# Kernel tuning notes

Measured on AMD Instinct MI355X. Metric: run time of the kernel, lower is better.

## Reference

```python
import jax, jax.numpy as jnp
import numpy as np

TAU = 0.2
ALPHA = 0.8
EPS = 1e-8  # torch cosine_similarity eps
LAM_POS = 1.5  # generate_lambda()=0.5, +1 for extrapolation
LAM_NEG = 0.5  # interpolation lambda


def _cos_sim_matrix(x):
    # row-normalize with clamped norm (matches F.cosine_similarity eps), then gram matrix
    n = x / jnp.maximum(jnp.linalg.norm(x, axis=1, keepdims=True), EPS)
    return n @ n.T


def setup_inputs() -> dict:
    key = jax.random.key(0)
    N, D = 4096, 512
    emb = jax.random.normal(key, (N, D), dtype=jnp.float32)
    # SimCLR-style symmetric positive pairs: (2k,2k+1) and (2k+1,2k)
    base = np.arange(0, N, 2)
    fwd_pairs = np.stack([base, base + 1], axis=1)
    pairs = np.concatenate([fwd_pairs, fwd_pairs[:, ::-1]], axis=0)  # [N, 2]
    return {"embeddings": emb, "positive_pairs": jnp.asarray(pairs, dtype=jnp.int32)}


def reference(embeddings, positive_pairs):
    # stage == 'train' (quantile-thresholded hard-negative branch)
    N = embeddings.shape[0]
    ar = jnp.arange(N)
    pi, pj = positive_pairs[:, 0], positive_pairs[:, 1]
    # ordered positive mask (symmetric because pairs include both orientations)
    pos_mask = jnp.zeros((N, N), dtype=bool).at[pi, pj].set(True)

    # --- extrapolate positive pairs: row i -> 1.5*e_i - 0.5*e_j ---
    partner_pos = jnp.full((N,), -1, dtype=jnp.int32).at[pi].set(pj.astype(jnp.int32))
    in_pair = partner_pos >= 0
    pp = jnp.where(in_pair, partner_pos, 0)
    hard_pos_emb = jnp.where(
        in_pair[:, None],
        LAM_POS * embeddings - (LAM_POS - 1.0) * embeddings[pp],
        embeddings,
    )

    # --- interpolate negative pairs: row k -> 0.5*(e_k + e_partner) ---
    # Negative pairs are all ordered (i,j), i!=j, not positive, scattered in
    # row k is the largest i with (i,k) negative.
    valid = (~pos_mask.T) & (ar[None, :] != ar[:, None])  # valid[k, i] = (i,k) is negative
    partner_neg = jnp.max(jnp.where(valid, ar[None, :], -1), axis=1)
    hard_neg_emb = LAM_NEG * embeddings + (1.0 - LAM_NEG) * embeddings[partner_neg]

    # --- three NxN cosine-sim matrices, composed by the scatter pattern ---
    orig_sim = _cos_sim_matrix(embeddings)
    hard_pos_sim = _cos_sim_matrix(hard_pos_emb)
    hard_neg_sim = _cos_sim_matrix(hard_neg_emb)
    diag = jnp.eye(N, dtype=bool)
    sim = jnp.where(diag, orig_sim, jnp.where(pos_mask, hard_pos_sim, hard_neg_sim))

    # --- contrastive loss with per-row quantile hard-negative threshold ---
    mask = diag | pos_mask
    exp_sim = jnp.exp(sim / TAU)
    exp_masked = jnp.where(mask, 0.0, exp_sim)
    pos_sim = exp_sim[pi, pj]              # [P]
    exp_rows = exp_masked[pi]              # [P, N]
    thr = jnp.quantile(exp_rows, ALPHA, axis=1, keepdims=True)
    hard_neg_sum = jnp.sum(jnp.where(exp_rows >= thr, exp_rows, 0.0), axis=1)
    loss = -jnp.log(pos_sim / (pos_sim + hard_neg_sum))
    # torch sums loss_ij + loss_ji over all rows / (2*P); with symmetric pair
    # list this equals sum(loss_ij)/P
    return jnp.sum(loss) / positive_pairs.shape[0]
```

## Files before the change

### kernel.cpp

```cpp
#include <hip/hip_runtime.h>
#include <cmath>

#define DIM 512
#define TAU_INV 5.0f
#define EPSN 1e-8f
#define ALPHA_Q 0.8f

typedef __attribute__((ext_vector_type(8))) unsigned short us8;
typedef __attribute__((ext_vector_type(4))) unsigned short us4;
typedef __attribute__((ext_vector_type(8))) short s8v;
typedef __attribute__((ext_vector_type(4))) float f4;

__device__ __forceinline__ unsigned short f2h(float f) {
    _Float16 h = (_Float16)f;
    return *(const unsigned short*)&h;
}
__device__ __forceinline__ float h2f(unsigned u) {
    unsigned short us = (unsigned short)u;
    _Float16 h = *(const _Float16*)&us;
    return (float)h;
}
__device__ __forceinline__ unsigned key16(unsigned u) {
    return u ^ (0x8000u | (0x7FFFu & (0u - (u >> 15))));
}
__device__ __forceinline__ float keyval(unsigned k) {
    unsigned u = (k & 0x8000u) ? (k & 0x7FFFu) : ((~k) & 0xFFFFu);
    return h2f(u);
}

__global__ void k_scatter(const int* __restrict__ pairs, int* partner, int P) {
    int k = blockIdx.x * 256 + threadIdx.x;
    if (k < P) partner[pairs[2 * k]] = pairs[2 * k + 1];
}
__global__ void k_pneg(const int* __restrict__ partner, int* pneg, int N) {
    int i = blockIdx.x * 256 + threadIdx.x;
    if (i >= N) return;
    int q = -1;
    for (int j = N - 1; j >= 0; --j) {
        if (j != i && partner[j] != i) { q = j; break; }
    }
    pneg[i] = q;
}

__global__ __launch_bounds__(128) void k_prep(const float* __restrict__ emb,
                                              const int* __restrict__ pneg,
                                              const int* __restrict__ pairs,
                                              unsigned short* __restrict__ mb,
                                              float* __restrict__ pos_term,
                                              int N, int P) {
    int bid = blockIdx.x, t = threadIdx.x;
    if (bid < N) {
        int i = bid;
        int q = pneg[i];
        float4 a = ((const float4*)(emb + (size_t)i * DIM))[t];
        float4 b = ((const float4*)(emb + (size_t)q * DIM))[t];
        float hx = 0.5f * (a.x + b.x), hy = 0.5f * (a.y + b.y);
        float hz = 0.5f * (a.z + b.z), hw = 0.5f * (a.w + b.w);
        float ss = hx * hx + hy * hy + hz * hz + hw * hw;
        for (int o = 32; o > 0; o >>= 1) ss += __shfl_down(ss, o);
        __shared__ float red[2];
        __shared__ float s_inv;
        if ((t & 63) == 0) red[t >> 6] = ss;
        __syncthreads();
        if (t == 0) s_inv = 1.0f / fmaxf(sqrtf(red[0] + red[1]), EPSN);
        __syncthreads();
        float inv = s_inv;
        us4 o4;
        o4[0] = f2h(hx * inv); o4[1] = f2h(hy * inv);
        o4[2] = f2h(hz * inv); o4[3] = f2h(hw * inv);
        *(us4*)(mb + (size_t)i * DIM + t * 4) = o4;
    } else {
        int k = bid - N;
        int i = pairs[2 * k], j = pairs[2 * k + 1];
        float4 a = ((const float4*)(emb + (size_t)i * DIM))[t];
        float4 b = ((const float4*)(emb + (size_t)j * DIM))[t];
        float dab = 0.f, naa = 0.f, nbb = 0.f;
        {
            float fa, fb;
            fa = 1.5f * a.x - 0.5f * b.x; fb = 1.5f * b.x - 0.5f * a.x; dab += fa * fb; naa += fa * fa; nbb += fb * fb;
            fa = 1.5f * a.y - 0.5f * b.y; fb = 1.5f * b.y - 0.5f * a.y; dab += fa * fb; naa += fa * fa; nbb += fb * fb;
            fa = 1.5f * a.z - 0.5f * b.z; fb = 1.5f * b.z - 0.5f * a.z; dab += fa * fb; naa += fa * fa; nbb += fb * fb;
            fa = 1.5f * a.w - 0.5f * b.w; fb = 1.5f * b.w - 0.5f * a.w; dab += fa * fb; naa += fa * fa; nbb += fb * fb;
        }
        for (int o = 32; o > 0; o >>= 1) {
            dab += __shfl_down(dab, o);
            naa += __shfl_down(naa, o);
            nbb += __shfl_down(nbb, o);
        }
        __shared__ float rd[2], ra[2], rb[2];
        if ((t & 63) == 0) { rd[t >> 6] = dab; ra[t >> 6] = naa; rb[t >> 6] = nbb; }
        __syncthreads();
        if (t == 0) {
            float d = rd[0] + rd[1], na = ra[0] + ra[1], nb = rb[0] + rb[1];
            float sim = d / (fmaxf(sqrtf(na), EPSN) * fmaxf(sqrtf(nb), EPSN));
            pos_term[k] = expf(sim * TAU_INV);
        }
    }
}

__global__ __launch_bounds__(256) void k_gemm(const unsigned short* __restrict__ mb,
                                              unsigned short* __restrict__ S, int N, int rowBase) {
    __shared__ __align__(16) unsigned short As[128][32];
    __shared__ __align__(16) unsigned short Bs[128][32];
    int tid = threadIdx.x;
    int wave = tid >> 6, lane = tid & 63, quad = lane >> 4, l16 = lane & 15;
    int wr = (wave >> 1) * 64, wc = (wave & 1) * 64;
    int iBase = rowBase + blockIdx.y * 128;
    int jBase = blockIdx.x * 128;
    int lrow = lane >> 2, lseg = lane & 3;

    const unsigned short* gA0 = mb + (size_t)(iBase + wave * 32 + lrow) * DIM + lseg * 8;
    const unsigned short* gA1 = gA0 + 16 * DIM;
    const unsigned short* gB0 = mb + (size_t)(jBase + wave * 32 + lrow) * DIM + lseg * 8;
    const unsigned short* gB1 = gB0 + 16 * DIM;
    __attribute__((address_space(3))) char* ldsA =
        (__attribute__((address_space(3))) char*)As + wave * 2048;
    __attribute__((address_space(3))) char* ldsB =
        (__attribute__((address_space(3))) char*)Bs + wave * 2048;

    f4 acc[4][4];
    for (int i = 0; i < 4; ++i)
        for (int j = 0; j < 4; ++j) acc[i][j] = (f4){0.f, 0.f, 0.f, 0.f};

    for (int k0 = 0; k0 < DIM; k0 += 32) {
        __syncthreads();
        __builtin_amdgcn_global_load_lds(
            (const __attribute__((address_space(1))) void*)(gA0 + k0),
            (__attribute__((address_space(3))) void*)(ldsA), 16, 0, 0);
        __builtin_amdgcn_global_load_lds(
            (const __attribute__((address_space(1))) void*)(gA1 + k0),
            (__attribute__((address_space(3))) void*)(ldsA + 1024), 16, 0, 0);
        __builtin_amdgcn_global_load_lds(
            (const __attribute__((address_space(1))) void*)(gB0 + k0),
            (__attribute__((address_space(3))) void*)(ldsB), 16, 0, 0);
        __builtin_amdgcn_global_load_lds(
            (const __attribute__((address_space(1))) void*)(gB1 + k0),
            (__attribute__((address_space(3))) void*)(ldsB + 1024), 16, 0, 0);
        __syncthreads();

        s8v a[4], b[4];
        for (int i = 0; i < 4; ++i) a[i] = *(const s8v*)&As[wr + i * 16 + l16][quad * 8];
        for (int j = 0; j < 4; ++j) b[j] = *(const s8v*)&Bs[wc + j * 16 + l16][quad * 8];
        for (int i = 0; i < 4; ++i)
            for (int j = 0; j < 4; ++j)
                acc[i][j] = __builtin_amdgcn_mfma_f32_16x16x32_f16(a[i], b[j], acc[i][j], 0, 0, 0);
    }
    int rQ = blockIdx.y * 128 + wr + quad * 4;
    int cQ = jBase + wc + l16;
    for (int i = 0; i < 4; ++i)
        for (int j = 0; j < 4; ++j)
            for (int rr = 0; rr < 4; ++rr)
                S[(size_t)(rQ + i * 16 + rr) * N + cQ + j * 16] = f2h(acc[i][j][rr]);
}

__global__ __launch_bounds__(256, 4) void k_select(const unsigned short* __restrict__ Sb,
                                                   const int* __restrict__ pairs,
                                                   const float* __restrict__ pos_term,
                                                   float* __restrict__ losses,
                                                   int N, int r0, int r1,
                                                   int klo, float frac) {
    __shared__ unsigned shcnt[2];
    __shared__ unsigned shmin;
    __shared__ float s_red[4];
    int tid = threadIdx.x, wid = tid >> 6, lane = tid & 63;
    int k = blockIdx.x;
    int row = pairs[2 * k];
    if (row < r0 || row >= r1) return;
    int pj = pairs[2 * k + 1];
    const us8* src8 = (const us8*)(Sb + (size_t)(row - r0) * N);

    us8 g0 = src8[tid];
    us8 g1 = src8[256 + tid];
    unsigned kr[16];
    {
        int m0 = row - tid * 8, p0 = pj - tid * 8;
        int m1 = row - 2048 - tid * 8, p1 = pj - 2048 - tid * 8;
        #pragma unroll
        for (int e = 0; e < 8; ++e) {
            unsigned u = (unsigned short)g0[e];
            kr[e] = ((e == m0) | (e == p0)) ? 0u : key16(u);
        }
        #pragma unroll
        for (int e = 0; e < 8; ++e) {
            unsigned u = (unsigned short)g1[e];
            kr[8 + e] = ((e == m1) | (e == p1)) ? 0u : key16(u);
        }
    }

    int nmask = (pj == row) ? 1 : 2;
    int Nreal = N - nmask;
    int Rreal = klo - nmask;
    float pos = pos_term[k];
    float s = 0.f;

    if (Rreal < 0) {
        #pragma unroll
        for (int e = 0; e < 16; ++e)
            if (kr[e] > 0u) s += __expf(keyval(kr[e]) * TAU_INV);
    } else {
        if (tid < 2) shcnt[tid] = 0u;
        if (tid == 0) shmin = 0xFFFFFFFFu;
        __syncthreads();
        int lim = Nreal - Rreal - 1;
        unsigned lo = 1, hi = 65535;
        int parity = 0;
        while (lo < hi) {
            unsigned mid = (lo + hi) >> 1;
            unsigned wcnt = 0;
            #pragma unroll
            for (int e = 0; e < 16; ++e)
                wcnt += (unsigned)__popcll(__ballot(kr[e] > mid));
            if (lane == 0) atomicAdd(&shcnt[parity], wcnt);
            __syncthreads();
            unsigned cnt = shcnt[parity];
            if (tid == 0) shcnt[parity ^ 1] = 0u;
            __syncthreads();
            if (cnt <= (unsigned)lim) hi = mid; else lo = mid + 1;
            parity ^= 1;
        }
        unsigned K1 = lo;

        if (frac > 1e-9f) {
            unsigned wcnt = 0, mymin = 0xFFFFFFFFu;
            #pragma unroll
            for (int e = 0; e < 16; ++e) {
                bool gt = kr[e] > K1;
                wcnt += (unsigned)__popcll(__ballot(gt));
                if (gt && kr[e] < mymin) mymin = kr[e];
            }
            for (int o = 1; o < 64; o <<= 1) {
                unsigned y = (unsigned)__shfl_xor((int)mymin, o);
                if (y < mymin) mymin = y;
            }
            if (lane == 0) {
                atomicAdd(&shcnt[parity], wcnt);
                atomicMin(&shmin, mymin);
            }
            __syncthreads();
            unsigned cntAbove = shcnt[parity];
            unsigned minAbove = shmin;
            unsigned K2;
            if (Rreal + 1 > Nreal - 1)                K2 = K1;
            else if (Nreal - (int)cntAbove >= Rreal + 2) K2 = K1;
            else                                      K2 = minAbove;
            float elo = __expf(keyval(K1) * TAU_INV);
            float ehi = __expf(keyval(K2) * TAU_INV);
            float thr = elo + frac * (ehi - elo);
            #pragma unroll
            for (int e = 0; e < 16; ++e) {
                if (kr[e] > 0u) {
                    float ev = __expf(keyval(kr[e]) * TAU_INV);
                    if (ev >= thr) s += ev;
                }
            }
        } else {
            #pragma unroll
            for (int e = 0; e < 16; ++e)
                if (kr[e] >= K1) s += __expf(keyval(kr[e]) * TAU_INV);
        }
    }

    for (int o = 1; o < 64; o <<= 1) s += __shfl_xor(s, o);
    if (lane == 0) s_red[wid] = s;
    __syncthreads();
    if (tid == 0) {
        float st = s_red[0] + s_red[1] + s_red[2] + s_red[3];
        losses[k] = logf((pos + st) / pos);
    }
}

__global__ __launch_bounds__(256) void k_reduce(const float* __restrict__ losses,
                                                float* __restrict__ out, int P, float invP) {
    __shared__ float s_red[4];
    int tid = threadIdx.x, wid = tid >> 6, lane = tid & 63;
    float s = 0.f;
    for (int i = tid; i < P; i += 256) s += losses[i];
    for (int o = 1; o < 64; o <<= 1) s += __shfl_xor(s, o);
    if (lane == 0) s_red[wid] = s;
    __syncthreads();
    if (tid == 0) out[0] = (s_red[0] + s_red[1] + s_red[2] + s_red[3]) * invP;
}

extern "C" void kernel_launch(void* const* d_in, const int* in_sizes, int n_in,
                              void* d_out, int out_size, void* d_ws, size_t ws_size,
                              hipStream_t stream) {
    const float* emb = (const float*)d_in[0];
    const int* pairs = (const int*)d_in[1];
    float* out = (float*)d_out;
    int N = in_sizes[0] / DIM;
    int P = in_sizes[1] / 2;

    char* ws = (char*)d_ws;
    size_t off = 0;
    unsigned short* mb = (unsigned short*)(ws + off); off += (size_t)N * DIM * 2;
    int* partner = (int*)(ws + off);                  off += (size_t)N * 4;
    int* pneg = (int*)(ws + off);                     off += (size_t)N * 4;
    float* pos_term = (float*)(ws + off);             off += (size_t)P * 4;
    float* losses = (float*)(ws + off);               off += (size_t)P * 4;
    off = (off + 255) & ~(size_t)255;
    unsigned short* Sbuf = (unsigned short*)(ws + off);
    size_t avail = (ws_size > off) ? ws_size - off : 0;
    long maxRows = (long)(avail / ((size_t)N * 2));
    int chunk = (int)(maxRows - (maxRows % 128));
    if (chunk > N) chunk = N;
    if (chunk < 128) chunk = 128;

    hipMemsetAsync(partner, 0xFF, (size_t)N * 4, stream);
    k_scatter<<<dim3((P + 255) / 256), dim3(256), 0, stream>>>(pairs, partner, P);
    k_pneg<<<dim3((N + 255) / 256), dim3(256), 0, stream>>>(partner, pneg, N);
    k_prep<<<dim3(N + P), dim3(128), 0, stream>>>(emb, pneg, pairs, mb, pos_term, N, P);

    float qpos = ALPHA_Q * (float)(N - 1);
    int klo = (int)floorf(qpos);
    float frac = qpos - (float)klo;
    float invP = 1.0f / (float)P;

    for (int r0 = 0; r0 < N; r0 += chunk) {
        int rows = (N - r0 < chunk) ? (N - r0) : chunk;
        dim3 g(N / 128, rows / 128);
        k_gemm<<<g, dim3(256), 0, stream>>>(mb, Sbuf, N, r0);
        k_select<<<dim3(P), dim3(256), 0, stream>>>(Sbuf, pairs, pos_term, losses,
                                                    N, r0, r0 + rows, klo, frac);
    }
    k_reduce<<<dim3(1), dim3(256), 0, stream>>>(losses, out, P, invP);
}
```

Measured before the change: 138.0 us.

## Exploit Gram matrix symmetry: compute upper-triangle tiles and write transposes via LDS

```diff
diff --git a/kernel.cpp b/kernel.cpp
--- a/kernel.cpp
+++ b/kernel.cpp
@@ -5,6 +5,7 @@
 #define TAU_INV 5.0f
 #define EPSN 1e-8f
 #define ALPHA_Q 0.8f
+#define TPITCH 72
 
 typedef __attribute__((ext_vector_type(8))) unsigned short us8;
 typedef __attribute__((ext_vector_type(4))) unsigned short us4;
@@ -94,6 +95,87 @@
             float d = rd[0] + rd[1], na = ra[0] + ra[1], nb = rb[0] + rb[1];
             float sim = d / (fmaxf(sqrtf(na), EPSN) * fmaxf(sqrtf(nb), EPSN));
             pos_term[k] = expf(sim * TAU_INV);
+        }
+    }
+}
+
+__global__ __launch_bounds__(256, 3) void k_gemm_sym(const unsigned short* __restrict__ mb,
+                                                     unsigned short* __restrict__ S, int N) {
+    __shared__ __align__(16) unsigned short As[128][32];
+    __shared__ __align__(16) unsigned short Bs[128][32];
+    __shared__ __align__(16) unsigned short Ts[4][64 * TPITCH];
+    int tid = threadIdx.x;
+    int wave = tid >> 6, lane = tid & 63, quad = lane >> 4, l16 = lane & 15;
+    int wr = (wave >> 1) * 64, wc = (wave & 1) * 64;
+
+    int ntb = N >> 7;
+    int bi = 0, rem = blockIdx.x, rowlen = ntb;
+    while (rem >= rowlen) { rem -= rowlen; ++bi; --rowlen; }
+    int bj = bi + rem;
+    int iBase = bi * 128, jBase = bj * 128;
+    int lrow = lane >> 2, lseg = lane & 3;
+
+    const unsigned short* gA0 = mb + (size_t)(iBase + wave * 32 + lrow) * DIM + lseg * 8;
+    const unsigned short* gA1 = gA0 + 16 * DIM;
+    const unsigned short* gB0 = mb + (size_t)(jBase + wave * 32 + lrow) * DIM + lseg * 8;
+    const unsigned short* gB1 = gB0 + 16 * DIM;
+    __attribute__((address_space(3))) char* ldsA =
+        (__attribute__((address_space(3))) char*)As + wave * 2048;
+    __attribute__((address_space(3))) char* ldsB =
+        (__attribute__((address_space(3))) char*)Bs + wave * 2048;
+
+    f4 acc[4][4];
+    for (int i = 0; i < 4; ++i)
+        for (int j = 0; j < 4; ++j) acc[i][j] = (f4){0.f, 0.f, 0.f, 0.f};
+
+    for (int k0 = 0; k0 < DIM; k0 += 32) {
+        __syncthreads();
+        __builtin_amdgcn_global_load_lds(
+            (const __attribute__((address_space(1))) void*)(gA0 + k0),
+            (__attribute__((address_space(3))) void*)(ldsA), 16, 0, 0);
+        __builtin_amdgcn_global_load_lds(
+            (const __attribute__((address_space(1))) void*)(gA1 + k0),
+            (__attribute__((address_space(3))) void*)(ldsA + 1024), 16, 0, 0);
+        __builtin_amdgcn_global_load_lds(
+            (const __attribute__((address_space(1))) void*)(gB0 + k0),
+            (__attribute__((address_space(3))) void*)(ldsB), 16, 0, 0);
+        __builtin_amdgcn_global_load_lds(
+            (const __attribute__((address_space(1))) void*)(gB1 + k0),
+            (__attribute__((address_space(3))) void*)(ldsB + 1024), 16, 0, 0);
+        __syncthreads();
+
+        s8v a[4], b[4];
+        for (int i = 0; i < 4; ++i) a[i] = *(const s8v*)&As[wr + i * 16 + l16][quad * 8];
+        for (int j = 0; j < 4; ++j) b[j] = *(const s8v*)&Bs[wc + j * 16 + l16][quad * 8];
+        for (int i = 0; i < 4; ++i)
+            for (int j = 0; j < 4; ++j)
+                acc[i][j] = __builtin_amdgcn_mfma_f32_16x16x32_f16(a[i], b[j], acc[i][j], 0, 0, 0);
+    }
+    int rQ = iBase + wr + quad * 4;
+    int cQ = jBase + wc + l16;
+    for (int i = 0; i < 4; ++i)
+        for (int j = 0; j < 4; ++j)
+            for (int rr = 0; rr < 4; ++rr)
+                S[(size_t)(rQ + i * 16 + rr) * N + cQ + j * 16] = f2h(acc[i][j][rr]);
+
+    if (bi != bj) {
+        unsigned short* T = &Ts[wave][0];
+        #pragma unroll
+        for (int i = 0; i < 4; ++i)
+            #pragma unroll
+            for (int j = 0; j < 4; ++j)
+                #pragma unroll
+                for (int rr = 0; rr < 4; ++rr) {
+                    int tr = quad * 4 + i * 16 + rr;
+                    int tc = l16 + j * 16;
+                    T[tc * TPITCH + tr] = f2h(acc[i][j][rr]);
+                }
+        int lrow8 = lane >> 3, lseg8 = lane & 7;
+        #pragma unroll
+        for (int it = 0; it < 8; ++it) {
+            int mr = it * 8 + lrow8;
+            us8 v = *(const us8*)&T[mr * TPITCH + lseg8 * 8];
+            *(us8*)&S[(size_t)(jBase + wc + mr) * N + iBase + wr + lseg8 * 8] = v;
         }
     }
 }
@@ -240,9 +322,9 @@
             unsigned cntAbove = shcnt[parity];
             unsigned minAbove = shmin;
             unsigned K2;
-            if (Rreal + 1 > Nreal - 1)                K2 = K1;
+            if (Rreal + 1 > Nreal - 1)                   K2 = K1;
             else if (Nreal - (int)cntAbove >= Rreal + 2) K2 = K1;
-            else                                      K2 = minAbove;
+            else                                         K2 = minAbove;
             float elo = __expf(keyval(K1) * TAU_INV);
             float ehi = __expf(keyval(K2) * TAU_INV);
             float thr = elo + frac * (ehi - elo);
@@ -315,12 +397,20 @@
     float frac = qpos - (float)klo;
     float invP = 1.0f / (float)P;
 
-    for (int r0 = 0; r0 < N; r0 += chunk) {
-        int rows = (N - r0 < chunk) ? (N - r0) : chunk;
-        dim3 g(N / 128, rows / 128);
-        k_gemm<<<g, dim3(256), 0, stream>>>(mb, Sbuf, N, r0);
+    if (chunk >= N) {
+        int ntb = N >> 7;
+        int nblk = ntb * (ntb + 1) / 2;
+        k_gemm_sym<<<dim3(nblk), dim3(256), 0, stream>>>(mb, Sbuf, N);
         k_select<<<dim3(P), dim3(256), 0, stream>>>(Sbuf, pairs, pos_term, losses,
-                                                    N, r0, r0 + rows, klo, frac);
+                                                    N, 0, N, klo, frac);
+    } else {
+        for (int r0 = 0; r0 < N; r0 += chunk) {
+            int rows = (N - r0 < chunk) ? (N - r0) : chunk;
+            dim3 g(N / 128, rows / 128);
+            k_gemm<<<g, dim3(256), 0, stream>>>(mb, Sbuf, N, r0);
+            k_select<<<dim3(P), dim3(256), 0, stream>>>(Sbuf, pairs, pos_term, losses,
+                                                        N, r0, r0 + rows, klo, frac);
+        }
     }
     k_reduce<<<dim3(1), dim3(256), 0, stream>>>(losses, out, P, invP);
 }
```

New measurement: 130.1 us. -5.8%, faster.
